# Kernel tuning notes

Measured on AMD Instinct MI355X. Metric: run time of the kernel, lower is better.

The kernel has to match this reference:

```python
import jax, jax.numpy as jnp
import numpy as np

K = 10        # n_functions (random MLP draws)
H = 20        # hidden width of each tiny per-feature MLP
LN_EPS = 1e-5 # torch LayerNorm default eps
STD_EPS = 1e-8


def _layernorm(h):
    # LayerNorm over last dim, affine weight=1, bias=0 (torch default init),
    # biased variance, eps=1e-5.
    mu = h.mean(-1, keepdims=True)
    var = ((h - mu) ** 2).mean(-1, keepdims=True)
    return (h - mu) * jax.lax.rsqrt(var + LN_EPS)


def setup_inputs() -> dict:
    key = jax.random.key(0)
    B, T, N = 128, 256, 16
    ks = jax.random.split(key, 7)
    inputs = jax.random.normal(ks[0], (B, T, N), dtype=jnp.float32)

    def u(k, shape, bound):
        return jax.random.uniform(k, shape, minval=-bound, maxval=bound, dtype=jnp.float32)

    # torch Linear default init: uniform(-1/sqrt(fan_in), 1/sqrt(fan_in)) for W and b
    W1 = u(ks[1], (K, N, H), 1.0)        # Linear(1,20): fan_in=1
    b1 = u(ks[2], (K, N, H), 1.0)
    bnd = 1.0 / np.sqrt(H)
    W2 = u(ks[3], (K, N, H, H), bnd)     # Linear(20,20), weight layout [out,in]
    b2 = u(ks[4], (K, N, H), bnd)
    W3 = u(ks[5], (K, N, H), bnd)        # Linear(20,1) weight squeezed to [H]
    b3 = u(ks[6], (K, N), bnd)
    return {"inputs": inputs, "W1": W1, "b1": b1, "W2": W2, "b2": b2, "W3": W3, "b3": b3}


def reference(inputs, W1, b1, W2, b2, W3, b3):
    x = inputs.astype(jnp.float32)
    # standardize over batch dim (torch .std is unbiased, ddof=1)
    x = (x - x.mean(0)) / x.std(0, ddof=1)

    # All K draws x all N per-feature MLPs as one batched computation.
    # h: [K, B, T, N, H]
    h = jax.nn.relu(x[None, ..., None] * W1[:, None, None] + b1[:, None, None])
    h = _layernorm(h)
    h = jax.nn.relu(jnp.einsum('kbtni,knoi->kbtno', h, W2) + b2[:, None, None])
    h = _layernorm(h)
    t = jnp.einsum('kbtni,kni->kbtn', h, W3) + b3[:, None, None]   # [K, B, T, N]

    # std_out: standardize over batch dim
    t = (t - t.mean(1, keepdims=True)) / (t.std(1, ddof=1, keepdims=True) + STD_EPS)

    m_marginals = t.mean(1)                   # [K, T, N]
    prod_marginals = jnp.prod(m_marginals, -1)  # [K, T]
    prod_joint = jnp.prod(t, -1).mean(1)        # [K, T]
    per_k_mse = jnp.mean((prod_marginals - prod_joint) ** 2, axis=-1)  # [K]
    return jnp.mean(per_k_mse)
```

## Files before the change

kernel.cpp:

```cpp
#include <hip/hip_runtime.h>
#include <math.h>

#define B_ 128
#define T_ 256
#define N_ 16
#define K_ 10
#define H_ 20
#define TN_ (T_ * N_)
#define S_ (T_ * B_)

__global__ void k_std(const float* __restrict__ x, float* __restrict__ xs2)
{
    const int tid = blockIdx.x * blockDim.x + threadIdx.x;
    const int tt = tid >> 4;
    const int n  = tid & 15;

    float sum = 0.f;
    for (int b = 0; b < B_; ++b) sum += x[b * TN_ + tid];
    const float mu = sum * (1.f / 128.f);

    float ss = 0.f;
    for (int b = 0; b < B_; ++b) {
        const float d = x[b * TN_ + tid] - mu;
        ss = fmaf(d, d, ss);
    }
    const float r = 1.f / sqrtf(ss * (1.f / 127.f));

    float* col = xs2 + ((size_t)n * T_ + tt) * B_;
    for (int b = 0; b < B_; b += 4) {
        float4 v;
        v.x = (x[(b + 0) * TN_ + tid] - mu) * r;
        v.y = (x[(b + 1) * TN_ + tid] - mu) * r;
        v.z = (x[(b + 2) * TN_ + tid] - mu) * r;
        v.w = (x[(b + 3) * TN_ + tid] - mu) * r;
        *reinterpret_cast<float4*>(col + b) = v;
    }
}

__global__ __launch_bounds__(256, 2) void k_mlp(
    const float* __restrict__ xs2,
    const float* __restrict__ W1, const float* __restrict__ b1,
    const float* __restrict__ W2, const float* __restrict__ b2,
    const float* __restrict__ W3, const float* __restrict__ b3,
    float* __restrict__ tb)
{
    const int kn  = blockIdx.y;
    const int k   = kn >> 4;
    const int n   = kn & 15;
    const int tid = threadIdx.x;

    __shared__ float sw1[H_], sb1[H_], sb2[H_], sw3[H_];
    __shared__ float sw2[H_ * H_];
    __shared__ float sb3s;

    if (tid < H_) {
        sw1[tid] = W1[kn * H_ + tid];
        sb1[tid] = b1[kn * H_ + tid];
        sb2[tid] = b2[kn * H_ + tid];
        sw3[tid] = W3[kn * H_ + tid];
    }
    for (int j = tid; j < H_ * H_; j += 256) sw2[j] = W2[kn * H_ * H_ + j];
    if (tid == 0) sb3s = b3[kn];
    __syncthreads();

    const int q0 = blockIdx.x * 1024 + tid;

    float u[4];
#pragma unroll
    for (int m = 0; m < 4; ++m) u[m] = xs2[n * S_ + q0 + m * 256];

    float h[4][H_];
#pragma unroll
    for (int m = 0; m < 4; ++m) {
        float s = 0.f;
#pragma unroll
        for (int i = 0; i < H_; ++i) {
            float a = fmaf(u[m], sw1[i], sb1[i]);
            a = fmaxf(a, 0.f);
            h[m][i] = a;
            s += a;
        }
        const float mu = s * (1.f / H_);
        float v = 0.f;
#pragma unroll
        for (int i = 0; i < H_; ++i) { const float d = h[m][i] - mu; v = fmaf(d, d, v); }
        const float r = 1.f / sqrtf(v * (1.f / H_) + 1e-5f);
#pragma unroll
        for (int i = 0; i < H_; ++i) h[m][i] = (h[m][i] - mu) * r;
    }

    float g[4][H_];
#pragma unroll
    for (int o = 0; o < H_; ++o) {
        float acc[4];
#pragma unroll
        for (int m = 0; m < 4; ++m) acc[m] = sb2[o];
#pragma unroll
        for (int i4 = 0; i4 < H_ / 4; ++i4) {
            const float4 w = *reinterpret_cast<const float4*>(&sw2[o * H_ + i4 * 4]);
            const int i = i4 * 4;
#pragma unroll
            for (int m = 0; m < 4; ++m) {
                acc[m] = fmaf(h[m][i + 0], w.x, acc[m]);
                acc[m] = fmaf(h[m][i + 1], w.y, acc[m]);
                acc[m] = fmaf(h[m][i + 2], w.z, acc[m]);
                acc[m] = fmaf(h[m][i + 3], w.w, acc[m]);
            }
        }
#pragma unroll
        for (int m = 0; m < 4; ++m) g[m][o] = fmaxf(acc[m], 0.f);
    }

#pragma unroll
    for (int m = 0; m < 4; ++m) {
        float s = 0.f;
#pragma unroll
        for (int i = 0; i < H_; ++i) s += g[m][i];
        const float mu = s * (1.f / H_);
        float v = 0.f;
#pragma unroll
        for (int i = 0; i < H_; ++i) { const float d = g[m][i] - mu; v = fmaf(d, d, v); }
        const float r = 1.f / sqrtf(v * (1.f / H_) + 1e-5f);

        float t = sb3s;
#pragma unroll
        for (int i = 0; i < H_; ++i) t = fmaf((g[m][i] - mu) * r, sw3[i], t);

        const int q  = q0 + m * 256;
        const int tt = q >> 7;
        const int b  = q & 127;
        tb[(((size_t)k * T_ + tt) * N_ + n) * B_ + b] = t;
    }
}

__global__ __launch_bounds__(128) void k_out(const float* __restrict__ tb,
                                             float* __restrict__ okt)
{
    __shared__ float s[N_ * B_];
    __shared__ float cm[N_];
    __shared__ float pjpart[2];

    const int kt  = blockIdx.x;
    const int tid = threadIdx.x;
    const int wv  = tid >> 6;
    const int l   = tid & 63;

    for (int j = tid; j < N_ * B_; j += 128)
        s[j] = tb[(size_t)kt * (N_ * B_) + j];
    __syncthreads();

    for (int c = 0; c < 8; ++c) {
        const int n = wv * 8 + c;
        const float a0 = s[n * B_ + l];
        const float a1 = s[n * B_ + 64 + l];

        float sm = a0 + a1;
#pragma unroll
        for (int off = 32; off; off >>= 1) sm += __shfl_xor(sm, off);
        const float mu = sm * (1.f / 128.f);

        const float d0 = a0 - mu, d1 = a1 - mu;
        float vv = fmaf(d0, d0, d1 * d1);
#pragma unroll
        for (int off = 32; off; off >>= 1) vv += __shfl_xor(vv, off);
        const float sd = sqrtf(vv * (1.f / 127.f));
        const float r  = 1.f / (sd + 1e-8f);

        const float z0 = d0 * r, z1 = d1 * r;
        s[n * B_ + l]      = z0;
        s[n * B_ + 64 + l] = z1;

        float zm = z0 + z1;
#pragma unroll
        for (int off = 32; off; off >>= 1) zm += __shfl_xor(zm, off);
        if (l == 0) cm[n] = zm * (1.f / 128.f);
    }
    __syncthreads();

    float pj = 1.f;
#pragma unroll
    for (int n = 0; n < N_; ++n) pj *= s[n * B_ + tid];
#pragma unroll
    for (int off = 32; off; off >>= 1) pj += __shfl_xor(pj, off);
    if (l == 0) pjpart[wv] = pj;
    __syncthreads();

    if (tid == 0) {
        const float pjm = (pjpart[0] + pjpart[1]) * (1.f / 128.f);
        float pm = 1.f;
        for (int n = 0; n < N_; ++n) pm *= cm[n];
        const float d = pm - pjm;
        okt[kt] = d * d;
    }
}

__global__ __launch_bounds__(256) void k_red(const float* __restrict__ okt,
                                             float* __restrict__ out)
{
    __shared__ double red[256];
    const int tid = threadIdx.x;
    double a = 0.0;
    for (int j = tid; j < K_ * T_; j += 256) a += (double)okt[j];
    red[tid] = a;
    __syncthreads();
    for (int stp = 128; stp; stp >>= 1) {
        if (tid < stp) red[tid] += red[tid + stp];
        __syncthreads();
    }
    if (tid == 0) out[0] = (float)(red[0] / (double)(K_ * T_));
}

extern "C" void kernel_launch(void* const* d_in, const int* in_sizes, int n_in,
                              void* d_out, int out_size, void* d_ws, size_t ws_size,
                              hipStream_t stream)
{
    const float* x  = (const float*)d_in[0];
    const float* W1 = (const float*)d_in[1];
    const float* b1 = (const float*)d_in[2];
    const float* W2 = (const float*)d_in[3];
    const float* b2 = (const float*)d_in[4];
    const float* W3 = (const float*)d_in[5];
    const float* b3 = (const float*)d_in[6];
    float* out = (float*)d_out;

    char* ws = (char*)d_ws;
    float* xs2 = (float*)ws;
    float* tb  = (float*)(ws + (size_t)2  * 1024 * 1024);
    float* okt = (float*)(ws + (size_t)23 * 1024 * 1024);

    k_std<<<TN_ / 256, 256, 0, stream>>>(x, xs2);

    dim3 g2(S_ / 1024, K_ * N_);
    k_mlp<<<g2, 256, 0, stream>>>(xs2, W1, b1, W2, b2, W3, b3, tb);

    k_out<<<K_ * T_, 128, 0, stream>>>(tb, okt);
    k_red<<<1, 256, 0, stream>>>(okt, out);
}
```

Before: 220.7 us.

## Rework all kernels: wave-per-column std, one sample per thread MLP, atomic final reduction

```diff
diff --git a/kernel.cpp b/kernel.cpp
--- a/kernel.cpp
+++ b/kernel.cpp
@@ -9,205 +9,136 @@
 #define TN_ (T_ * N_)
 #define S_ (T_ * B_)
 
-__global__ void k_std(const float* __restrict__ x, float* __restrict__ xs2)
+__device__ __forceinline__ float wsum(float v)
 {
-    const int tid = blockIdx.x * blockDim.x + threadIdx.x;
-    const int tt = tid >> 4;
-    const int n  = tid & 15;
+#pragma unroll
+    for (int off = 32; off; off >>= 1) v += __shfl_xor(v, off);
+    return v;
+}
 
-    float sum = 0.f;
-    for (int b = 0; b < B_; ++b) sum += x[b * TN_ + tid];
-    const float mu = sum * (1.f / 128.f);
+__global__ __launch_bounds__(256) void k_std(const float* __restrict__ x,
+                                             float* __restrict__ xs2)
+{
+    const int wid = (blockIdx.x * 256 + threadIdx.x) >> 6;
+    const int l   = threadIdx.x & 63;
+    const int tt  = wid >> 4;
+    const int n   = wid & 15;
 
-    float ss = 0.f;
-    for (int b = 0; b < B_; ++b) {
-        const float d = x[b * TN_ + tid] - mu;
-        ss = fmaf(d, d, ss);
-    }
-    const float r = 1.f / sqrtf(ss * (1.f / 127.f));
+    const float a0 = x[l * TN_ + wid];
+    const float a1 = x[(64 + l) * TN_ + wid];
+
+    const float sm = wsum(a0 + a1);
+    const float mu = sm * (1.f / 128.f);
+
+    const float d0 = a0 - mu, d1 = a1 - mu;
+    const float vv = wsum(fmaf(d0, d0, d1 * d1));
+    const float r  = __builtin_amdgcn_rsqf(vv * (1.f / 127.f));
 
     float* col = xs2 + ((size_t)n * T_ + tt) * B_;
-    for (int b = 0; b < B_; b += 4) {
-        float4 v;
-        v.x = (x[(b + 0) * TN_ + tid] - mu) * r;
-        v.y = (x[(b + 1) * TN_ + tid] - mu) * r;
-        v.z = (x[(b + 2) * TN_ + tid] - mu) * r;
-        v.w = (x[(b + 3) * TN_ + tid] - mu) * r;
-        *reinterpret_cast<float4*>(col + b) = v;
-    }
+    col[l]      = d0 * r;
+    col[64 + l] = d1 * r;
 }
 
-__global__ __launch_bounds__(256, 2) void k_mlp(
+__global__ __launch_bounds__(256) void k_mlp(
     const float* __restrict__ xs2,
     const float* __restrict__ W1, const float* __restrict__ b1,
     const float* __restrict__ W2, const float* __restrict__ b2,
     const float* __restrict__ W3, const float* __restrict__ b3,
     float* __restrict__ tb)
 {
-    const int kn  = blockIdx.y;
-    const int k   = kn >> 4;
-    const int n   = kn & 15;
-    const int tid = threadIdx.x;
+    const int kn = blockIdx.y;
+    const int n  = kn & 15;
 
-    __shared__ float sw1[H_], sb1[H_], sb2[H_], sw3[H_];
-    __shared__ float sw2[H_ * H_];
-    __shared__ float sb3s;
+    const float* __restrict__ w1  = W1 + kn * H_;
+    const float* __restrict__ bb1 = b1 + kn * H_;
+    const float* __restrict__ w2  = W2 + kn * H_ * H_;
+    const float* __restrict__ bb2 = b2 + kn * H_;
+    const float* __restrict__ w3  = W3 + kn * H_;
+    const float  bb3 = b3[kn];
 
-    if (tid < H_) {
-        sw1[tid] = W1[kn * H_ + tid];
-        sb1[tid] = b1[kn * H_ + tid];
-        sb2[tid] = b2[kn * H_ + tid];
-        sw3[tid] = W3[kn * H_ + tid];
+    const int q = blockIdx.x * 256 + threadIdx.x;
+    const float u = xs2[n * S_ + q];
+
+    float h[H_];
+    float s = 0.f;
+#pragma unroll
+    for (int i = 0; i < H_; ++i) {
+        const float a = fmaxf(fmaf(u, w1[i], bb1[i]), 0.f);
+        h[i] = a; s += a;
     }
-    for (int j = tid; j < H_ * H_; j += 256) sw2[j] = W2[kn * H_ * H_ + j];
-    if (tid == 0) sb3s = b3[kn];
-    __syncthreads();
+    const float mu = s * (1.f / H_);
+    float v = 0.f;
+#pragma unroll
+    for (int i = 0; i < H_; ++i) { const float d = h[i] - mu; v = fmaf(d, d, v); }
+    const float r  = __builtin_amdgcn_rsqf(v * (1.f / H_) + 1e-5f);
+    const float mr = mu * r;
+#pragma unroll
+    for (int i = 0; i < H_; ++i) h[i] = fmaf(h[i], r, -mr);
 
-    const int q0 = blockIdx.x * 1024 + tid;
-
-    float u[4];
+    float g[H_];
+    float s2 = 0.f;
 #pragma unroll
-    for (int m = 0; m < 4; ++m) u[m] = xs2[n * S_ + q0 + m * 256];
-
-    float h[4][H_];
+    for (int o = 0; o < H_; ++o) {
+        float acc = bb2[o];
 #pragma unroll
-    for (int m = 0; m < 4; ++m) {
-        float s = 0.f;
-#pragma unroll
-        for (int i = 0; i < H_; ++i) {
-            float a = fmaf(u[m], sw1[i], sb1[i]);
-            a = fmaxf(a, 0.f);
-            h[m][i] = a;
-            s += a;
-        }
-        const float mu = s * (1.f / H_);
-        float v = 0.f;
-#pragma unroll
-        for (int i = 0; i < H_; ++i) { const float d = h[m][i] - mu; v = fmaf(d, d, v); }
-        const float r = 1.f / sqrtf(v * (1.f / H_) + 1e-5f);
-#pragma unroll
-        for (int i = 0; i < H_; ++i) h[m][i] = (h[m][i] - mu) * r;
+        for (int i = 0; i < H_; ++i) acc = fmaf(h[i], w2[o * H_ + i], acc);
+        acc = fmaxf(acc, 0.f);
+        g[o] = acc; s2 += acc;
     }
 
-    float g[4][H_];
+    const float mu2 = s2 * (1.f / H_);
+    float v2 = 0.f;
 #pragma unroll
-    for (int o = 0; o < H_; ++o) {
-        float acc[4];
+    for (int o = 0; o < H_; ++o) { const float d = g[o] - mu2; v2 = fmaf(d, d, v2); }
+    const float r2  = __builtin_amdgcn_rsqf(v2 * (1.f / H_) + 1e-5f);
+    const float mr2 = mu2 * r2;
+
+    float t = bb3;
 #pragma unroll
-        for (int m = 0; m < 4; ++m) acc[m] = sb2[o];
+    for (int o = 0; o < H_; ++o) t = fmaf(fmaf(g[o], r2, -mr2), w3[o], t);
+
+    const int tt = q >> 7;
+    const int b  = q & 127;
+    tb[(((size_t)kn >> 4) * T_ + tt) * (N_ * B_) + n * B_ + b] = t;
+}
+
+__global__ __launch_bounds__(256) void k_out(const float* __restrict__ tb,
+                                             float* __restrict__ out)
+{
+    const int gw = (blockIdx.x * 256 + threadIdx.x) >> 6;
+    const int l  = threadIdx.x & 63;
+    const float* base = tb + (size_t)gw * (N_ * B_);
+
+    float z0[N_], z1[N_], cm[N_];
 #pragma unroll
-        for (int i4 = 0; i4 < H_ / 4; ++i4) {
-            const float4 w = *reinterpret_cast<const float4*>(&sw2[o * H_ + i4 * 4]);
-            const int i = i4 * 4;
+    for (int n = 0; n < N_; ++n) {
+        z0[n] = base[n * B_ + l];
+        z1[n] = base[n * B_ + 64 + l];
+    }
 #pragma unroll
-            for (int m = 0; m < 4; ++m) {
-                acc[m] = fmaf(h[m][i + 0], w.x, acc[m]);
-                acc[m] = fmaf(h[m][i + 1], w.y, acc[m]);
-                acc[m] = fmaf(h[m][i + 2], w.z, acc[m]);
-                acc[m] = fmaf(h[m][i + 3], w.w, acc[m]);
-            }
-        }
-#pragma unroll
-        for (int m = 0; m < 4; ++m) g[m][o] = fmaxf(acc[m], 0.f);
+    for (int n = 0; n < N_; ++n) {
+        const float sm = wsum(z0[n] + z1[n]);
+        const float mu = sm * (1.f / 128.f);
+        const float d0 = z0[n] - mu, d1 = z1[n] - mu;
+        const float vv = wsum(fmaf(d0, d0, d1 * d1));
+        const float sd = sqrtf(vv * (1.f / 127.f));
+        const float rr = 1.f / (sd + 1e-8f);
+        z0[n] = d0 * rr; z1[n] = d1 * rr;
+        cm[n] = wsum(z0[n] + z1[n]) * (1.f / 128.f);
     }
 
+    float p0 = 1.f, p1 = 1.f;
 #pragma unroll
-    for (int m = 0; m < 4; ++m) {
-        float s = 0.f;
+    for (int n = 0; n < N_; ++n) { p0 *= z0[n]; p1 *= z1[n]; }
+    const float pj = wsum(p0 + p1) * (1.f / 128.f);
+
+    if (l == 0) {
+        float pm = 1.f;
 #pragma unroll
-        for (int i = 0; i < H_; ++i) s += g[m][i];
-        const float mu = s * (1.f / H_);
-        float v = 0.f;
-#pragma unroll
-        for (int i = 0; i < H_; ++i) { const float d = g[m][i] - mu; v = fmaf(d, d, v); }
-        const float r = 1.f / sqrtf(v * (1.f / H_) + 1e-5f);
-
-        float t = sb3s;
-#pragma unroll
-        for (int i = 0; i < H_; ++i) t = fmaf((g[m][i] - mu) * r, sw3[i], t);
-
-        const int q  = q0 + m * 256;
-        const int tt = q >> 7;
-        const int b  = q & 127;
-        tb[(((size_t)k * T_ + tt) * N_ + n) * B_ + b] = t;
+        for (int n = 0; n < N_; ++n) pm *= cm[n];
+        const float d = pm - pj;
+        atomicAdd(out, d * d * (1.f / (K_ * T_)));
     }
-}
-
-__global__ __launch_bounds__(128) void k_out(const float* __restrict__ tb,
-                                             float* __restrict__ okt)
-{
-    __shared__ float s[N_ * B_];
-    __shared__ float cm[N_];
-    __shared__ float pjpart[2];
-
-    const int kt  = blockIdx.x;
-    const int tid = threadIdx.x;
-    const int wv  = tid >> 6;
-    const int l   = tid & 63;
-
-    for (int j = tid; j < N_ * B_; j += 128)
-        s[j] = tb[(size_t)kt * (N_ * B_) + j];
-    __syncthreads();
-
-    for (int c = 0; c < 8; ++c) {
-        const int n = wv * 8 + c;
-        const float a0 = s[n * B_ + l];
-        const float a1 = s[n * B_ + 64 + l];
-
-        float sm = a0 + a1;
-#pragma unroll
-        for (int off = 32; off; off >>= 1) sm += __shfl_xor(sm, off);
-        const float mu = sm * (1.f / 128.f);
-
-        const float d0 = a0 - mu, d1 = a1 - mu;
-        float vv = fmaf(d0, d0, d1 * d1);
-#pragma unroll
-        for (int off = 32; off; off >>= 1) vv += __shfl_xor(vv, off);
-        const float sd = sqrtf(vv * (1.f / 127.f));
-        const float r  = 1.f / (sd + 1e-8f);
-
-        const float z0 = d0 * r, z1 = d1 * r;
-        s[n * B_ + l]      = z0;
-        s[n * B_ + 64 + l] = z1;
-
-        float zm = z0 + z1;
-#pragma unroll
-        for (int off = 32; off; off >>= 1) zm += __shfl_xor(zm, off);
-        if (l == 0) cm[n] = zm * (1.f / 128.f);
-    }
-    __syncthreads();
-
-    float pj = 1.f;
-#pragma unroll
-    for (int n = 0; n < N_; ++n) pj *= s[n * B_ + tid];
-#pragma unroll
-    for (int off = 32; off; off >>= 1) pj += __shfl_xor(pj, off);
-    if (l == 0) pjpart[wv] = pj;
-    __syncthreads();
-
-    if (tid == 0) {
-        const float pjm = (pjpart[0] + pjpart[1]) * (1.f / 128.f);
-        float pm = 1.f;
-        for (int n = 0; n < N_; ++n) pm *= cm[n];
-        const float d = pm - pjm;
-        okt[kt] = d * d;
-    }
-}
-
-__global__ __launch_bounds__(256) void k_red(const float* __restrict__ okt,
-                                             float* __restrict__ out)
-{
-    __shared__ double red[256];
-    const int tid = threadIdx.x;
-    double a = 0.0;
-    for (int j = tid; j < K_ * T_; j += 256) a += (double)okt[j];
-    red[tid] = a;
-    __syncthreads();
-    for (int stp = 128; stp; stp >>= 1) {
-        if (tid < stp) red[tid] += red[tid + stp];
-        __syncthreads();
-    }
-    if (tid == 0) out[0] = (float)(red[0] / (double)(K_ * T_));
 }
 
 extern "C" void kernel_launch(void* const* d_in, const int* in_sizes, int n_in,
@@ -225,14 +156,14 @@
 
     char* ws = (char*)d_ws;
     float* xs2 = (float*)ws;
-    float* tb  = (float*)(ws + (size_t)2  * 1024 * 1024);
-    float* okt = (float*)(ws + (size_t)23 * 1024 * 1024);
+    float* tb  = (float*)(ws + (size_t)2 * 1024 * 1024);
 
-    k_std<<<TN_ / 256, 256, 0, stream>>>(x, xs2);
+    hipMemsetAsync(out, 0, sizeof(float), stream);
 
-    dim3 g2(S_ / 1024, K_ * N_);
+    k_std<<<(TN_ * 64) / 256, 256, 0, stream>>>(x, xs2);
+
+    dim3 g2(S_ / 256, K_ * N_);
     k_mlp<<<g2, 256, 0, stream>>>(xs2, W1, b1, W2, b2, W3, b3, tb);
 
-    k_out<<<K_ * T_, 128, 0, stream>>>(tb, okt);
-    k_red<<<1, 256, 0, stream>>>(okt, out);
+    k_out<<<(K_ * T_ * 64) / 256, 256, 0, stream>>>(tb, out);
 }
```

Result: faster. 203.0 us (-8.1%).
